# Kernel optimization log

Measured on AMD Instinct MI355X. Metric: run time of the kernel, lower is better.

Reference implementation:

```python
import jax, jax.numpy as jnp
import numpy as np

B, T, D = 64, 512, 512
H, DH = 8, 64  # head_num, att_embedding_size; H*DH == D
NEG = jnp.float32(-2.0**32 + 1)


def _pos_encoding(t, d):
    # Position_Embedding (mode='sum'): [cos, sin] concat over d/2 frequencies
    inv_freq = 1.0 / jnp.power(10000.0, 2.0 * jnp.arange(d // 2, dtype=jnp.float32) / d)
    pij = jnp.arange(t, dtype=jnp.float32)[:, None] * inv_freq[None, :]  # (T, d/2)
    return jnp.concatenate([jnp.cos(pij), jnp.sin(pij)], axis=-1)  # (T, d)


def setup_inputs() -> dict:
    key = jax.random.key(0)
    ks = jax.random.split(key, 9)
    queries = jax.random.normal(ks[0], (B, T, D), dtype=jnp.float32)
    keys = jax.random.normal(ks[1], (B, T, D), dtype=jnp.float32)
    query_lens = jax.random.randint(ks[2], (B, 1), 1, T + 1)
    key_lens = jax.random.randint(ks[3], (B, 1), 1, T + 1)
    W_Q = jax.random.truncated_normal(ks[4], -2., 2., (D, H * DH), dtype=jnp.float32) * 0.05
    W_K = jax.random.truncated_normal(ks[5], -2., 2., (D, H * DH), dtype=jnp.float32) * 0.05
    W_V = jax.random.truncated_normal(ks[6], -2., 2., (D, H * DH), dtype=jnp.float32) * 0.05
    fw1 = jax.random.normal(ks[7], (H * DH, 4 * H * DH), dtype=jnp.float32) * 0.02
    fw2 = jax.random.normal(ks[8], (4 * H * DH, H * DH), dtype=jnp.float32) * 0.02
    return {"queries": queries, "keys": keys, "query_lens": query_lens,
            "key_lens": key_lens, "W_Q": W_Q, "W_K": W_K, "W_V": W_V,
            "fw1": fw1, "fw2": fw2}


def reference(queries, keys, query_lens, key_lens, W_Q, W_K, W_V, fw1, fw2):
    # sequence masks (B, T) from lengths (B, 1)
    ar = jnp.arange(T)
    q_mask = (ar[None, :] < query_lens).astype(jnp.float32)  # (B, T)
    k_mask = ar[None, :] < key_lens                          # (B, T) bool

    pe = _pos_encoding(T, D)[None]  # (1, T, D)
    q_in = queries + pe
    k_in = keys + pe

    qp = jnp.einsum('btd,de->bte', q_in, W_Q).reshape(B, T, H, DH)
    kp = jnp.einsum('btd,de->bte', k_in, W_K)
    # DeepCTR quirk: values projected from the already-projected keys
    vp = jnp.einsum('btd,de->bte', kp, W_V).reshape(B, T, H, DH)
    kp = kp.reshape(B, T, H, DH)

    scores = jnp.einsum('bthd,bshd->bhts', qp, kp) / jnp.sqrt(jnp.float32(DH))
    scores = jnp.where(k_mask[:, None, None, :], scores, NEG)
    scores = scores - jnp.max(scores, axis=-1, keepdims=True)
    attn = jax.nn.softmax(scores, axis=-1)
    attn = attn * q_mask[:, None, :, None]

    out = jnp.einsum('bhts,bshd->bthd', attn, vp).reshape(B, T, H * DH)
    result = out + q_in  # residual uses PE-augmented queries

    ff = jnp.einsum('btd,df->btf', jax.nn.relu(jnp.einsum('btd,df->btf', result, fw1)), fw2)
    result = result + ff

    return jnp.mean(result, axis=1, keepdims=True)  # (B, 1, D)
```

## Files before the change

### kernel.cpp

```cpp
#include <hip/hip_runtime.h>

typedef unsigned short u16;
typedef __attribute__((ext_vector_type(8))) short short8;
typedef __attribute__((ext_vector_type(4))) float floatx4;

#define QSCALE 0.1803368801111204f

__device__ __forceinline__ u16 f2bf(float x) {
  union { float f; unsigned u; } un; un.f = x;
  unsigned r = un.u + 0x7fffu + ((un.u >> 16) & 1u);
  return (u16)(r >> 16);
}
__device__ __forceinline__ float bf2f(u16 h) {
  union { unsigned u; float f; } un; un.u = ((unsigned)h) << 16;
  return un.f;
}
__device__ __forceinline__ void gld16(const u16* g, u16* l) {
  __builtin_amdgcn_global_load_lds((__attribute__((address_space(1))) void*)g,
                                   (__attribute__((address_space(3))) void*)l, 16, 0, 0);
}

__global__ __launch_bounds__(256) void wtrans_all(const float* __restrict__ W_Q,
                                                  const float* __restrict__ W_K,
                                                  const float* __restrict__ fw1,
                                                  u16* __restrict__ WqT, u16* __restrict__ WkT,
                                                  u16* __restrict__ F1T) {
  __shared__ float tile[32][33];
  int L = blockIdx.x;
  const float* in;
  u16* out;
  int N, bx, by;
  if (L < 256) { in = W_Q; out = WqT; N = 512; bx = L & 15; by = L >> 4; }
  else if (L < 512) { L -= 256; in = W_K; out = WkT; N = 512; bx = L & 15; by = L >> 4; }
  else { L -= 512; in = fw1; out = F1T; N = 2048; bx = L & 63; by = L >> 6; }
  int tx = threadIdx.x, ty = threadIdx.y;
  int n0 = bx * 32, k0 = by * 32;
#pragma unroll
  for (int i = 0; i < 4; i++) {
    int kk = ty + i * 8;
    tile[kk][tx] = in[(size_t)(k0 + kk) * N + n0 + tx];
  }
  __syncthreads();
#pragma unroll
  for (int i = 0; i < 4; i++) {
    int nn = ty + i * 8;
    out[(size_t)(n0 + nn) * 512 + k0 + tx] = f2bf(tile[tx][nn]);
  }
}

__global__ __launch_bounds__(256) void wkv_kernel(const float* __restrict__ WK,
                                                  const float* __restrict__ WV,
                                                  u16* __restrict__ WkvT) {
  __shared__ float Kt[32][36];
  __shared__ float Vt[32][36];
  int nt = blockIdx.x & 15, dt = blockIdx.x >> 4;
  int n0 = nt * 32, d0 = dt * 32;
  int tid = threadIdx.x;
  int flat = tid * 4;
  int i4 = flat >> 5, j4 = flat & 31;
  int tn = tid & 15, td = tid >> 4;
  float acc00 = 0.f, acc01 = 0.f, acc10 = 0.f, acc11 = 0.f;
  for (int e0 = 0; e0 < 512; e0 += 32) {
    __syncthreads();
    *(float4*)&Kt[i4][j4] = *(const float4*)&WK[(size_t)(d0 + i4) * 512 + e0 + j4];
    *(float4*)&Vt[i4][j4] = *(const float4*)&WV[(size_t)(e0 + i4) * 512 + n0 + j4];
    __syncthreads();
#pragma unroll 8
    for (int e = 0; e < 32; e++) {
      float k0v = Kt[td * 2][e], k1v = Kt[td * 2 + 1][e];
      float v0 = Vt[e][tn * 2], v1 = Vt[e][tn * 2 + 1];
      acc00 += k0v * v0; acc01 += k0v * v1;
      acc10 += k1v * v0; acc11 += k1v * v1;
    }
  }
  size_t o = (size_t)(n0 + tn * 2) * 512 + d0 + td * 2;
  WkvT[o] = f2bf(acc00);
  WkvT[o + 1] = f2bf(acc10);
  WkvT[o + 512] = f2bf(acc01);
  WkvT[o + 513] = f2bf(acc11);
}

__global__ __launch_bounds__(256) void pe_table_kernel(float* __restrict__ pet) {
  int flat = (blockIdx.x * 256 + threadIdx.x) * 4;
  int d0 = flat & 511;
  int t = flat >> 9;
  float pe[4];
#pragma unroll
  for (int i = 0; i < 4; i++) {
    int d = d0 + i;
    int j = (d < 256) ? d : d - 256;
    float f = exp2f((float)j * -0.05190512648f);
    float arg = (float)t * f;
    pe[i] = (d < 256) ? cosf(arg) : sinf(arg);
  }
  *(float4*)(pet + flat) = *(const float4*)pe;
}

__global__ __launch_bounds__(256) void pe_add_kernel(const float* __restrict__ q,
                                                     const float* __restrict__ k,
                                                     const float* __restrict__ pet,
                                                     u16* __restrict__ qb, u16* __restrict__ kb) {
  size_t flat = ((size_t)blockIdx.x * 256 + threadIdx.x) * 4;
  const float4 qv = *(const float4*)(q + flat);
  const float4 kv = *(const float4*)(k + flat);
  const float4 pv = *(const float4*)(pet + (flat & 262143));
  u16 qo[4], ko[4];
  qo[0] = f2bf(qv.x + pv.x); qo[1] = f2bf(qv.y + pv.y);
  qo[2] = f2bf(qv.z + pv.z); qo[3] = f2bf(qv.w + pv.w);
  ko[0] = f2bf(kv.x + pv.x); ko[1] = f2bf(kv.y + pv.y);
  ko[2] = f2bf(kv.z + pv.z); ko[3] = f2bf(kv.w + pv.w);
  *(uint2*)(qb + flat) = *(const uint2*)qo;
  *(uint2*)(kb + flat) = *(const uint2*)ko;
}

template <int HT>
__device__ __forceinline__ void stage_half(const u16* M, int tbase, int k0, u16* buf,
                                           int w, int lane) {
  const int srow = lane >> 3;
  const int sg = (lane & 7) ^ srow;
#pragma unroll
  for (int i = 0; i < 2; i++) {
    int j = w * 2 + i;
    int row0;
    if constexpr (HT == 0) row0 = j * 8 + ((j >= 8) ? 64 : 0);
    else if constexpr (HT == 3) row0 = j * 8 + ((j >= 8) ? 64 : 0) + 64;
    else if constexpr (HT == 1) row0 = (j >> 2) * 64 + (j & 3) * 8;
    else row0 = (j >> 2) * 64 + 32 + (j & 3) * 8;
    gld16(M + ((size_t)(tbase + row0 + srow) * 512 + k0 + sg * 8), &buf[row0 * 64]);
  }
}

__device__ __forceinline__ void kloop256(const u16* __restrict__ A, const u16* __restrict__ Bt,
                                         int tm, int tn, u16* lds, int tid,
                                         floatx4 (&acc)[8][4]) {
  const int lane = tid & 63, w = tid >> 6;
  const int quad = lane >> 4, cl = lane & 15;
  const int wm = w >> 2, wn = w & 3;
  const int nk = 8;

  stage_half<0>(A, tm, 0, lds, w, lane);
  stage_half<1>(Bt, tn, 0, lds + 16384, w, lane);
  stage_half<2>(Bt, tn, 0, lds + 16384, w, lane);
  stage_half<3>(A, tm, 0, lds, w, lane);
  asm volatile("s_waitcnt vmcnt(4)" ::: "memory");
  __builtin_amdgcn_s_barrier();

#pragma unroll 1
  for (int kt = 0; kt < nk; kt++) {
    u16* Ab = lds + (kt & 1) * 32768;
    u16* Bb = Ab + 16384;
    u16* An = lds + ((kt & 1) ^ 1) * 32768;
    u16* Bn = An + 16384;
    const bool pf = (kt + 1 < nk);
    const int k0n = (kt + 1) << 6;
    short8 a0[4][2], a1[4][2], b0[2][2], b1[2][2];

#pragma unroll
    for (int f = 0; f < 4; f++)
#pragma unroll
      for (int kh = 0; kh < 2; kh++)
        a0[f][kh] = *(const short8*)&Ab[(wm * 128 + f * 16 + cl) * 64 + ((((kh << 2) + quad)) ^ (cl & 7)) * 8];
#pragma unroll
    for (int n = 0; n < 2; n++)
#pragma unroll
      for (int kh = 0; kh < 2; kh++)
        b0[n][kh] = *(const short8*)&Bb[(wn * 64 + n * 16 + cl) * 64 + ((((kh << 2) + quad)) ^ (cl & 7)) * 8];
    if (pf) {
      stage_half<0>(A, tm, k0n, An, w, lane);
      asm volatile("s_waitcnt vmcnt(4)" ::: "memory");
    } else {
      asm volatile("s_waitcnt vmcnt(2)" ::: "memory");
    }
    __builtin_amdgcn_s_barrier();
    asm volatile("s_waitcnt lgkmcnt(0)" ::: "memory");
    __builtin_amdgcn_sched_barrier(0);
    __builtin_amdgcn_s_setprio(1);
#pragma unroll
    for (int f = 0; f < 4; f++)
#pragma unroll
      for (int n = 0; n < 2; n++)
#pragma unroll
        for (int kh = 0; kh < 2; kh++)
          acc[f][n] = __builtin_amdgcn_mfma_f32_16x16x32_bf16(a0[f][kh], b0[n][kh], acc[f][n], 0, 0, 0);
    __builtin_amdgcn_s_setprio(0);
    __builtin_amdgcn_s_barrier();

#pragma unroll
    for (int n = 0; n < 2; n++)
#pragma unroll
      for (int kh = 0; kh < 2; kh++)
        b1[n][kh] = *(const short8*)&Bb[(wn * 64 + (n + 2) * 16 + cl) * 64 + ((((kh << 2) + quad)) ^ (cl & 7)) * 8];
    if (pf) {
      stage_half<1>(Bt, tn, k0n, Bn, w, lane);
      asm volatile("s_waitcnt vmcnt(4)" ::: "memory");
    } else {
      asm volatile("s_waitcnt vmcnt(0)" ::: "memory");
    }
    __builtin_amdgcn_s_barrier();
    asm volatile("s_waitcnt lgkmcnt(0)" ::: "memory");
    __builtin_amdgcn_sched_barrier(0);
    __builtin_amdgcn_s_setprio(1);
#pragma unroll
    for (int f = 0; f < 4; f++)
#pragma unroll
      for (int n = 0; n < 2; n++)
#pragma unroll
        for (int kh = 0; kh < 2; kh++)
          acc[f][n + 2] = __builtin_amdgcn_mfma_f32_16x16x32_bf16(a0[f][kh], b1[n][kh], acc[f][n + 2], 0, 0, 0);
    __builtin_amdgcn_s_setprio(0);
    __builtin_amdgcn_s_barrier();

#pragma unroll
    for (int f = 0; f < 4; f++)
#pragma unroll
      for (int kh = 0; kh < 2; kh++)
        a1[f][kh] = *(const short8*)&Ab[(wm * 128 + (f + 4) * 16 + cl) * 64 + ((((kh << 2) + quad)) ^ (cl & 7)) * 8];
    if (pf) stage_half<2>(Bt, tn, k0n, Bn, w, lane);
    __builtin_amdgcn_s_barrier();
    asm volatile("s_waitcnt lgkmcnt(0)" ::: "memory");
    __builtin_amdgcn_sched_barrier(0);
    __builtin_amdgcn_s_setprio(1);
#pragma unroll
    for (int f = 0; f < 4; f++)
#pragma unroll
      for (int n = 0; n < 2; n++)
#pragma unroll
        for (int kh = 0; kh < 2; kh++)
          acc[f + 4][n + 2] = __builtin_amdgcn_mfma_f32_16x16x32_bf16(a1[f][kh], b1[n][kh], acc[f + 4][n + 2], 0, 0, 0);
    __builtin_amdgcn_s_setprio(0);
    __builtin_amdgcn_s_barrier();

    if (pf) {
      stage_half<3>(A, tm, k0n, An, w, lane);
      asm volatile("s_waitcnt vmcnt(4)" ::: "memory");
    }
    __builtin_amdgcn_s_barrier();
    __builtin_amdgcn_s_setprio(1);
#pragma unroll
    for (int f = 0; f < 4; f++)
#pragma unroll
      for (int n = 0; n < 2; n++)
#pragma unroll
        for (int kh = 0; kh < 2; kh++)
          acc[f + 4][n] = __builtin_amdgcn_mfma_f32_16x16x32_bf16(a1[f][kh], b0[n][kh], acc[f + 4][n], 0, 0, 0);
    __builtin_amdgcn_s_setprio(0);
    __builtin_amdgcn_s_barrier();
  }
}

__global__ __launch_bounds__(512, 2) void proj_256(const u16* __restrict__ q_in,
                                                   const u16* __restrict__ k_in,
                                                   const u16* __restrict__ WqT,
                                                   const u16* __restrict__ WkT,
                                                   const u16* __restrict__ WkvT,
                                                   u16* __restrict__ qp,
                                                   u16* __restrict__ kpb,
                                                   u16* __restrict__ vTp) {
  __shared__ u16 lds[65536];
  const int tid = threadIdx.x;
  const int lane = tid & 63, w = tid >> 6;
  const int quad = lane >> 4, cl = lane & 15;
  const int wm = w >> 2, wn = w & 3;
  int L = blockIdx.x;
  const int seg = L >> 8;
  L &= 255;
  const u16* A = (seg == 0) ? q_in : k_in;
  const u16* Bt = (seg == 0) ? WqT : (seg == 1) ? WkT : WkvT;
  const int xcd = L & 7, s = L >> 3;
  const int nx = s & 1;
  const int rgrp = s >> 1;
  const int tm = (rgrp * 8 + xcd) * 256;
  const int tn = nx * 256;

  floatx4 acc[8][4] = {};
  kloop256(A, Bt, tm, tn, lds, tid, acc);

  if (seg < 2) {
    u16* C = (seg == 0) ? qp : kpb;
#pragma unroll
    for (int f = 0; f < 8; f++)
#pragma unroll
      for (int n = 0; n < 4; n++)
#pragma unroll
        for (int r = 0; r < 4; r++) {
          int row = tm + wm * 128 + f * 16 + quad * 4 + r;
          int col = tn + wn * 64 + n * 16 + cl;
          C[(size_t)row * 512 + col] = f2bf(acc[f][n][r]);
        }
  } else {
    const int b = tm >> 9, sbase = tm & 511;
#pragma unroll 1
    for (int p = 0; p < 2; p++) {
      __syncthreads();
      if ((wn >> 1) == p) {
        int cbase = (wn & 1) * 64;
#pragma unroll
        for (int f = 0; f < 8; f++)
#pragma unroll
          for (int n = 0; n < 4; n++)
#pragma unroll
            for (int r = 0; r < 4; r++) {
              int tc = cbase + n * 16 + cl;
              int row = wm * 128 + f * 16 + quad * 4 + r;
              lds[tc * 264 + row] = f2bf(acc[f][n][r]);
            }
      }
      __syncthreads();
      int col = tid >> 2;
      int e = tn + p * 128 + col;
      int h = e >> 6, d = e & 63;
      u16* dst = vTp + ((size_t)((b * 8 + h) * 64 + d) * 512 + sbase);
#pragma unroll
      for (int j = 0; j < 8; j++) {
        int chunk = (tid & 3) + j * 4;
        *(short8*)(dst + chunk * 8) = *(const short8*)&lds[col * 264 + chunk * 8];
      }
    }
  }
}

__global__ __launch_bounds__(512, 2) void ffn1_256(const u16* __restrict__ A,
                                                   const u16* __restrict__ Bt,
                                                   float* __restrict__ outp) {
  __shared__ u16 lds[65536];
  const int tid = threadIdx.x;
  const int lane = tid & 63, w = tid >> 6;
  const int quad = lane >> 4, cl = lane & 15;
  const int wn = w & 3;
  int L = blockIdx.x;
  const int xcd = L & 7, s = L >> 3;
  const int nx = s & 7;
  const int rgrp = s >> 3;
  const int tm = (rgrp * 8 + xcd) * 256;
  const int tn = nx * 256;

  floatx4 acc[8][4] = {};
  kloop256(A, Bt, tm, tn, lds, tid, acc);

  float cs[4] = {0.f, 0.f, 0.f, 0.f};
#pragma unroll
  for (int f = 0; f < 8; f++)
#pragma unroll
    for (int n = 0; n < 4; n++)
#pragma unroll
      for (int r = 0; r < 4; r++) cs[n] += fmaxf(acc[f][n][r], 0.0f);
#pragma unroll
  for (int n = 0; n < 4; n++) {
    cs[n] += __shfl_xor(cs[n], 16);
    cs[n] += __shfl_xor(cs[n], 32);
  }
  if (quad == 0) {
    int b = tm >> 9;
#pragma unroll
    for (int n = 0; n < 4; n++)
      atomicAdd(outp + (size_t)b * 2048 + tn + wn * 64 + n * 16 + cl, cs[n]);
  }
}

__global__ __launch_bounds__(256) void ffn2_mean_kernel(const float* __restrict__ sums,
                                                        const float* __restrict__ fw2,
                                                        float* __restrict__ outp) {
  __shared__ float s[128];
  int fs = blockIdx.x & 15, b = blockIdx.x >> 4;
  int tid = threadIdx.x;
  if (tid < 128) s[tid] = sums[(size_t)b * 2048 + fs * 128 + tid];
  __syncthreads();
  const float* w = fw2 + (size_t)(fs * 128) * 512;
  float a0 = 0.f, a1 = 0.f;
#pragma unroll 4
  for (int f = 0; f < 128; f++) {
    float sv = s[f];
    a0 += sv * w[(size_t)f * 512 + tid];
    a1 += sv * w[(size_t)f * 512 + 256 + tid];
  }
  atomicAdd(outp + b * 512 + tid, a0 * (1.0f / 512.0f));
  atomicAdd(outp + b * 512 + 256 + tid, a1 * (1.0f / 512.0f));
}

__global__ __launch_bounds__(256) void attn_kernel(const u16* __restrict__ qp, const u16* __restrict__ kp,
                                                   const u16* __restrict__ vT, const u16* __restrict__ qin,
                                                   u16* __restrict__ resout, const int* __restrict__ qlen,
                                                   const int* __restrict__ klen, float* __restrict__ outp) {
  __shared__ u16 KPu[8704];
  __shared__ u16 Vlds[64 * 128];
  __shared__ float Csum[4][64];
  int L = blockIdx.x;
  int xcd = L & 7;
  int idx = L >> 3;
  int qt = idx & 7;
  int g = xcd + (idx >> 3) * 8;
  int h = g & 7, b = g >> 3;
  int tid = threadIdx.x, lane = tid & 63, w = tid >> 6;
  int quad = lane >> 4, cl = lane & 15;
  int kl = klen[b], ql = qlen[b];
  int q0 = qt * 64 + w * 16;

  if (qt * 64 >= ql) {
    int c = tid & 63, r0 = (tid >> 6) * 16;
    float sv = 0.f;
#pragma unroll
    for (int i = 0; i < 16; i++) {
      size_t idx2 = ((size_t)(b * 512 + qt * 64 + r0 + i) * 512) + h * 64 + c;
      u16 val = qin[idx2];
      resout[idx2] = val;
      sv += bf2f(val);
    }
    Csum[w][c] = sv;
    __syncthreads();
    if (tid < 64) {
      float t = Csum[0][tid] + Csum[1][tid] + Csum[2][tid] + Csum[3][tid];
      atomicAdd(outp + b * 512 + h * 64 + tid, t * (1.0f / 512.0f));
    }
    return;
  }
  bool wactive = q0 < ql;

  short8 qfrag[2];
#pragma unroll
  for (int ks = 0; ks < 2; ks++)
    qfrag[ks] = *(const short8*)(qp + ((size_t)(b * 512 + q0 + cl) * 512 + h * 64 + ks * 32 + quad * 8));
  const short8 ones8 = {(short)0x3F80, (short)0x3F80, (short)0x3F80, (short)0x3F80,
                        (short)0x3F80, (short)0x3F80, (short)0x3F80, (short)0x3F80};
  float m_r[4];
  floatx4 o[4] = {};
  floatx4 lacc = {};
#pragma unroll
  for (int r = 0; r < 4; r++) m_r[r] = -3.0e38f;

  int nkt = (kl + 127) >> 7;
  for (int kt = 0; kt < nkt; kt++) {
    __syncthreads();
#pragma unroll
    for (int i = 0; i < 4; i++) {
      int c = w * 4 + i;
      int row = c * 8 + (lane >> 3);
      int gc = (lane & 7) ^ (row & 7);
      gld16(kp + ((size_t)(b * 512 + kt * 128 + row) * 512 + h * 64 + gc * 8), &KPu[c * 512]);
    }
#pragma unroll
    for (int i = 0; i < 4; i++) {
      int c = w * 4 + i;
      int row = c * 4 + (lane >> 4);
      int gc = (lane & 15) ^ (row & 7);
      gld16(vT + ((size_t)((b * 8 + h) * 64 + row) * 512 + kt * 128 + gc * 8), &Vlds[c * 512]);
    }
    asm volatile("s_waitcnt vmcnt(4)" ::: "memory");
    __builtin_amdgcn_s_barrier();
    __builtin_amdgcn_sched_barrier(0);
    floatx4 sacc[8] = {};
    float mnew[4], alpha[4];
    if (wactive) {
      __builtin_amdgcn_s_setprio(1);
#pragma unroll
      for (int f = 0; f < 8; f++) {
        int krow = f * 16 + cl;
#pragma unroll
        for (int ks = 0; ks < 2; ks++) {
          int kc = ks * 4 + quad;
          short8 kf = *(const short8*)&KPu[krow * 64 + ((kc ^ (cl & 7)) * 8)];
          sacc[f] = __builtin_amdgcn_mfma_f32_16x16x32_bf16(qfrag[ks], kf, sacc[f], 0, 0, 0);
        }
      }
      __builtin_amdgcn_s_setprio(0);
#pragma unroll
      for (int r = 0; r < 4; r++) mnew[r] = m_r[r];
#pragma unroll
      for (int f = 0; f < 8; f++) {
        int key = kt * 128 + f * 16 + cl;
        bool ok = key < kl;
#pragma unroll
        for (int r = 0; r < 4; r++) {
          float v = ok ? sacc[f][r] * QSCALE : -4294967296.0f;
          sacc[f][r] = v;
          mnew[r] = fmaxf(mnew[r], v);
        }
      }
#pragma unroll
      for (int mk = 1; mk <= 8; mk <<= 1)
#pragma unroll
        for (int r = 0; r < 4; r++) mnew[r] = fmaxf(mnew[r], __shfl_xor(mnew[r], mk));
#pragma unroll
      for (int r = 0; r < 4; r++) {
        alpha[r] = exp2f(m_r[r] - mnew[r]);
        m_r[r] = mnew[r];
      }
    }
    __syncthreads();
    if (wactive) {
      u16* P = &KPu[w * 2176];
#pragma unroll
      for (int f = 0; f < 8; f++)
#pragma unroll
        for (int r = 0; r < 4; r++) {
          float p = exp2f(sacc[f][r] - mnew[r]);
          P[(quad * 4 + r) * 136 + f * 16 + cl] = f2bf(p);
        }
#pragma unroll
      for (int r = 0; r < 4; r++) lacc[r] *= alpha[r];
#pragma unroll
      for (int fd = 0; fd < 4; fd++)
#pragma unroll
        for (int r = 0; r < 4; r++) o[fd][r] *= alpha[r];
      __builtin_amdgcn_s_setprio(1);
#pragma unroll
      for (int k2 = 0; k2 < 4; k2++) {
        short8 pf = *(const short8*)&P[cl * 136 + k2 * 32 + quad * 8];
        lacc = __builtin_amdgcn_mfma_f32_16x16x32_bf16(pf, ones8, lacc, 0, 0, 0);
#pragma unroll
        for (int fd = 0; fd < 4; fd++) {
          int vrow = fd * 16 + cl;
          int sc = k2 * 4 + quad;
          short8 vf = *(const short8*)&Vlds[vrow * 128 + ((sc ^ (cl & 7)) * 8)];
          o[fd] = __builtin_amdgcn_mfma_f32_16x16x32_bf16(pf, vf, o[fd], 0, 0, 0);
        }
      }
      __builtin_amdgcn_s_setprio(0);
    }
  }
  float colsum[4] = {0.f, 0.f, 0.f, 0.f};
#pragma unroll
  for (int fd = 0; fd < 4; fd++)
#pragma unroll
    for (int r = 0; r < 4; r++) {
      int q = q0 + quad * 4 + r;
      float v = o[fd][r] / lacc[r];
      if (q >= ql) v = 0.f;
      size_t idx2 = (size_t)(b * 512 + q) * 512 + h * 64 + fd * 16 + cl;
      v += bf2f(qin[idx2]);
      resout[idx2] = f2bf(v);
      colsum[fd] += v;
    }
#pragma unroll
  for (int fd = 0; fd < 4; fd++) {
    colsum[fd] += __shfl_xor(colsum[fd], 16);
    colsum[fd] += __shfl_xor(colsum[fd], 32);
  }
  if (quad == 0) {
#pragma unroll
    for (int fd = 0; fd < 4; fd++) Csum[w][fd * 16 + cl] = colsum[fd];
  }
  __syncthreads();
  if (tid < 64) {
    float t = Csum[0][tid] + Csum[1][tid] + Csum[2][tid] + Csum[3][tid];
    atomicAdd(outp + b * 512 + h * 64 + tid, t * (1.0f / 512.0f));
  }
}

extern "C" void kernel_launch(void* const* d_in, const int* in_sizes, int n_in,
                              void* d_out, int out_size, void* d_ws, size_t ws_size,
                              hipStream_t stream) {
  const float* queries = (const float*)d_in[0];
  const float* keys = (const float*)d_in[1];
  const int* qlen = (const int*)d_in[2];
  const int* klen = (const int*)d_in[3];
  const float* W_Q = (const float*)d_in[4];
  const float* W_K = (const float*)d_in[5];
  const float* W_V = (const float*)d_in[6];
  const float* fw1 = (const float*)d_in[7];
  const float* fw2 = (const float*)d_in[8];
  float* outp = (float*)d_out;
  char* ws = (char*)d_ws;

  constexpr size_t SZ_W = 512 * 512 * 2;
  constexpr size_t SZ_F = 2048 * 512 * 2;
  constexpr size_t SZ_S = 64 * 2048 * 4;
  constexpr size_t SZ_T = (size_t)64 * 512 * 512 * 2;
  size_t o_WqT = 0;
  size_t o_WkT = o_WqT + SZ_W;
  size_t o_Wkv = o_WkT + SZ_W;
  size_t o_F1T = o_Wkv + SZ_W;
  size_t o_SUM = o_F1T + SZ_F;
  size_t o_ABCD = o_SUM + SZ_S;
  size_t o_E = o_ABCD + 4 * SZ_T;
  size_t NEED = o_E + SZ_T;
  if (ws_size < NEED) return;

  u16* WqT = (u16*)(ws + o_WqT);
  u16* WkT = (u16*)(ws + o_WkT);
  u16* WkvT = (u16*)(ws + o_Wkv);
  u16* F1T = (u16*)(ws + o_F1T);
  float* sums = (float*)(ws + o_SUM);
  u16* q_in = (u16*)(ws + o_ABCD);
  u16* k_in = (u16*)(ws + o_ABCD + SZ_T);
  u16* qp = (u16*)(ws + o_ABCD + 2 * SZ_T);
  u16* kpb = (u16*)(ws + o_ABCD + 3 * SZ_T);
  u16* vT = (u16*)(ws + o_E);
  float* pet = (float*)(ws + o_E);
  u16* resb = k_in;

  hipMemsetAsync(d_out, 0, (size_t)out_size * sizeof(float), stream);
  hipMemsetAsync(sums, 0, SZ_S, stream);

  wtrans_all<<<1536, dim3(32, 8), 0, stream>>>(W_Q, W_K, fw1, WqT, WkT, F1T);
  wkv_kernel<<<256, 256, 0, stream>>>(W_K, W_V, WkvT);
  pe_table_kernel<<<256, 256, 0, stream>>>(pet);
  pe_add_kernel<<<16384, 256, 0, stream>>>(queries, keys, pet, q_in, k_in);

  proj_256<<<768, 512, 0, stream>>>(q_in, k_in, WqT, WkT, WkvT, qp, kpb, vT);

  attn_kernel<<<4096, 256, 0, stream>>>(qp, kpb, vT, q_in, resb, qlen, klen, outp);

  ffn1_256<<<1024, 512, 0, stream>>>(resb, F1T, sums);
  ffn2_mean_kernel<<<1024, 256, 0, stream>>>(sums, fw2, outp);
}
```

Baseline: 397.0 us.

## Merge prep kernels, simplify GEMM pipeline, replace atomics with deterministic reductions

Folds the weight transpose, Wk·Wv product and positional table into one prep kernel, cutting launches. The two memsets go away because attention and ffn1 now write per-tile partial sums to dedicated slots instead of accumulating with atomics. A single ffn2_final kernel reduces those slots, multiplies by fw2 and writes the output directly. The GEMM k-loop is restructured to prefetch the whole next A/B tile at once, dropping the staged quarter-loads and setprio. The cost is fewer barriers overlapping loads with MFMA, and a 64-block final kernel with little parallelism.

```diff
diff --git a/kernel.cpp b/kernel.cpp
--- a/kernel.cpp
+++ b/kernel.cpp
@@ -20,80 +20,80 @@
                                    (__attribute__((address_space(3))) void*)l, 16, 0, 0);
 }
 
-__global__ __launch_bounds__(256) void wtrans_all(const float* __restrict__ W_Q,
-                                                  const float* __restrict__ W_K,
-                                                  const float* __restrict__ fw1,
-                                                  u16* __restrict__ WqT, u16* __restrict__ WkT,
-                                                  u16* __restrict__ F1T) {
-  __shared__ float tile[32][33];
+__global__ __launch_bounds__(256) void prep_kernel(const float* __restrict__ W_Q,
+                                                   const float* __restrict__ W_K,
+                                                   const float* __restrict__ W_V,
+                                                   const float* __restrict__ fw1,
+                                                   u16* __restrict__ WqT, u16* __restrict__ WkT,
+                                                   u16* __restrict__ F1T, u16* __restrict__ WkvT,
+                                                   float* __restrict__ pet) {
   int L = blockIdx.x;
-  const float* in;
-  u16* out;
-  int N, bx, by;
-  if (L < 256) { in = W_Q; out = WqT; N = 512; bx = L & 15; by = L >> 4; }
-  else if (L < 512) { L -= 256; in = W_K; out = WkT; N = 512; bx = L & 15; by = L >> 4; }
-  else { L -= 512; in = fw1; out = F1T; N = 2048; bx = L & 63; by = L >> 6; }
-  int tx = threadIdx.x, ty = threadIdx.y;
-  int n0 = bx * 32, k0 = by * 32;
-#pragma unroll
-  for (int i = 0; i < 4; i++) {
-    int kk = ty + i * 8;
-    tile[kk][tx] = in[(size_t)(k0 + kk) * N + n0 + tx];
-  }
-  __syncthreads();
-#pragma unroll
-  for (int i = 0; i < 4; i++) {
-    int nn = ty + i * 8;
-    out[(size_t)(n0 + nn) * 512 + k0 + tx] = f2bf(tile[tx][nn]);
-  }
-}
-
-__global__ __launch_bounds__(256) void wkv_kernel(const float* __restrict__ WK,
-                                                  const float* __restrict__ WV,
-                                                  u16* __restrict__ WkvT) {
-  __shared__ float Kt[32][36];
-  __shared__ float Vt[32][36];
-  int nt = blockIdx.x & 15, dt = blockIdx.x >> 4;
-  int n0 = nt * 32, d0 = dt * 32;
-  int tid = threadIdx.x;
-  int flat = tid * 4;
-  int i4 = flat >> 5, j4 = flat & 31;
-  int tn = tid & 15, td = tid >> 4;
-  float acc00 = 0.f, acc01 = 0.f, acc10 = 0.f, acc11 = 0.f;
-  for (int e0 = 0; e0 < 512; e0 += 32) {
+  int tid = threadIdx.y * 32 + threadIdx.x;
+  if (L < 1536) {
+    __shared__ float tile[32][33];
+    const float* in;
+    u16* out;
+    int N, bx, by;
+    if (L < 256) { in = W_Q; out = WqT; N = 512; bx = L & 15; by = L >> 4; }
+    else if (L < 512) { L -= 256; in = W_K; out = WkT; N = 512; bx = L & 15; by = L >> 4; }
+    else { L -= 512; in = fw1; out = F1T; N = 2048; bx = L & 63; by = L >> 6; }
+    int tx = threadIdx.x, ty = threadIdx.y;
+    int n0 = bx * 32, k0 = by * 32;
+#pragma unroll
+    for (int i = 0; i < 4; i++) {
+      int kk = ty + i * 8;
+      tile[kk][tx] = in[(size_t)(k0 + kk) * N + n0 + tx];
+    }
     __syncthreads();
-    *(float4*)&Kt[i4][j4] = *(const float4*)&WK[(size_t)(d0 + i4) * 512 + e0 + j4];
-    *(float4*)&Vt[i4][j4] = *(const float4*)&WV[(size_t)(e0 + i4) * 512 + n0 + j4];
-    __syncthreads();
+#pragma unroll
+    for (int i = 0; i < 4; i++) {
+      int nn = ty + i * 8;
+      out[(size_t)(n0 + nn) * 512 + k0 + tx] = f2bf(tile[tx][nn]);
+    }
+  } else if (L < 1792) {
+    L -= 1536;
+    __shared__ float Kt[32][36];
+    __shared__ float Vt[32][36];
+    int nt = L & 15, dt = L >> 4;
+    int n0 = nt * 32, d0 = dt * 32;
+    int flat = tid * 4;
+    int i4 = flat >> 5, j4 = flat & 31;
+    int tn = tid & 15, td = tid >> 4;
+    float acc00 = 0.f, acc01 = 0.f, acc10 = 0.f, acc11 = 0.f;
+    for (int e0 = 0; e0 < 512; e0 += 32) {
+      __syncthreads();
+      *(float4*)&Kt[i4][j4] = *(const float4*)&W_K[(size_t)(d0 + i4) * 512 + e0 + j4];
+      *(float4*)&Vt[i4][j4] = *(const float4*)&W_V[(size_t)(e0 + i4) * 512 + n0 + j4];
+      __syncthreads();
 #pragma unroll 8
-    for (int e = 0; e < 32; e++) {
-      float k0v = Kt[td * 2][e], k1v = Kt[td * 2 + 1][e];
-      float v0 = Vt[e][tn * 2], v1 = Vt[e][tn * 2 + 1];
-      acc00 += k0v * v0; acc01 += k0v * v1;
-      acc10 += k1v * v0; acc11 += k1v * v1;
-    }
-  }
-  size_t o = (size_t)(n0 + tn * 2) * 512 + d0 + td * 2;
-  WkvT[o] = f2bf(acc00);
-  WkvT[o + 1] = f2bf(acc10);
-  WkvT[o + 512] = f2bf(acc01);
-  WkvT[o + 513] = f2bf(acc11);
-}
-
-__global__ __launch_bounds__(256) void pe_table_kernel(float* __restrict__ pet) {
-  int flat = (blockIdx.x * 256 + threadIdx.x) * 4;
-  int d0 = flat & 511;
-  int t = flat >> 9;
-  float pe[4];
-#pragma unroll
-  for (int i = 0; i < 4; i++) {
-    int d = d0 + i;
-    int j = (d < 256) ? d : d - 256;
-    float f = exp2f((float)j * -0.05190512648f);
-    float arg = (float)t * f;
-    pe[i] = (d < 256) ? cosf(arg) : sinf(arg);
-  }
-  *(float4*)(pet + flat) = *(const float4*)pe;
+      for (int e = 0; e < 32; e++) {
+        float k0v = Kt[td * 2][e], k1v = Kt[td * 2 + 1][e];
+        float v0 = Vt[e][tn * 2], v1 = Vt[e][tn * 2 + 1];
+        acc00 += k0v * v0; acc01 += k0v * v1;
+        acc10 += k1v * v0; acc11 += k1v * v1;
+      }
+    }
+    size_t o = (size_t)(n0 + tn * 2) * 512 + d0 + td * 2;
+    WkvT[o] = f2bf(acc00);
+    WkvT[o + 1] = f2bf(acc10);
+    WkvT[o + 512] = f2bf(acc01);
+    WkvT[o + 513] = f2bf(acc11);
+  } else {
+    L -= 1792;
+    int flat = (L * 256 + tid) * 4;
+    int d0 = flat & 511;
+    int t = flat >> 9;
+    float pe[4];
+#pragma unroll
+    for (int i = 0; i < 4; i++) {
+      int d = d0 + i;
+      int j = (d < 256) ? d : d - 256;
+      float f = exp2f((float)j * -0.05190512648f);
+      float arg = (float)t * f;
+      pe[i] = (d < 256) ? cosf(arg) : sinf(arg);
+    }
+    *(float4*)(pet + flat) = *(const float4*)pe;
+  }
 }
 
 __global__ __launch_bounds__(256) void pe_add_kernel(const float* __restrict__ q,
@@ -113,38 +113,33 @@
   *(uint2*)(kb + flat) = *(const uint2*)ko;
 }
 
-template <int HT>
-__device__ __forceinline__ void stage_half(const u16* M, int tbase, int k0, u16* buf,
-                                           int w, int lane) {
-  const int srow = lane >> 3;
-  const int sg = (lane & 7) ^ srow;
-#pragma unroll
-  for (int i = 0; i < 2; i++) {
-    int j = w * 2 + i;
-    int row0;
-    if constexpr (HT == 0) row0 = j * 8 + ((j >= 8) ? 64 : 0);
-    else if constexpr (HT == 3) row0 = j * 8 + ((j >= 8) ? 64 : 0) + 64;
-    else if constexpr (HT == 1) row0 = (j >> 2) * 64 + (j & 3) * 8;
-    else row0 = (j >> 2) * 64 + 32 + (j & 3) * 8;
-    gld16(M + ((size_t)(tbase + row0 + srow) * 512 + k0 + sg * 8), &buf[row0 * 64]);
-  }
-}
-
 __device__ __forceinline__ void kloop256(const u16* __restrict__ A, const u16* __restrict__ Bt,
                                          int tm, int tn, u16* lds, int tid,
                                          floatx4 (&acc)[8][4]) {
+  const int K = 512;
   const int lane = tid & 63, w = tid >> 6;
   const int quad = lane >> 4, cl = lane & 15;
   const int wm = w >> 2, wn = w & 3;
-  const int nk = 8;
-
-  stage_half<0>(A, tm, 0, lds, w, lane);
-  stage_half<1>(Bt, tn, 0, lds + 16384, w, lane);
-  stage_half<2>(Bt, tn, 0, lds + 16384, w, lane);
-  stage_half<3>(A, tm, 0, lds, w, lane);
-  asm volatile("s_waitcnt vmcnt(4)" ::: "memory");
-  __builtin_amdgcn_s_barrier();
-
+  const int srow = lane >> 3;
+  const int sg = (lane & 7) ^ srow;
+  const int cb = w * 4;
+
+  {
+    u16* Ab = lds;
+    u16* Bb = lds + 16384;
+#pragma unroll
+    for (int i = 0; i < 4; i++) {
+      int cc = cb + i, row = cc * 8 + srow;
+      gld16(A + ((size_t)(tm + row) * K + sg * 8), &Ab[cc * 512]);
+    }
+#pragma unroll
+    for (int i = 0; i < 4; i++) {
+      int cc = cb + i, row = cc * 8 + srow;
+      gld16(Bt + ((size_t)(tn + row) * K + sg * 8), &Bb[cc * 512]);
+    }
+  }
+
+  const int nk = K >> 6;
 #pragma unroll 1
   for (int kt = 0; kt < nk; kt++) {
     u16* Ab = lds + (kt & 1) * 32768;
@@ -153,8 +148,24 @@
     u16* Bn = An + 16384;
     const bool pf = (kt + 1 < nk);
     const int k0n = (kt + 1) << 6;
-    short8 a0[4][2], a1[4][2], b0[2][2], b1[2][2];
-
+    if (pf) {
+#pragma unroll
+      for (int i = 0; i < 4; i++) {
+        int cc = cb + i, row = cc * 8 + srow;
+        gld16(A + ((size_t)(tm + row) * K + k0n + sg * 8), &An[cc * 512]);
+      }
+#pragma unroll
+      for (int i = 0; i < 4; i++) {
+        int cc = cb + i, row = cc * 8 + srow;
+        gld16(Bt + ((size_t)(tn + row) * K + k0n + sg * 8), &Bn[cc * 512]);
+      }
+      asm volatile("s_waitcnt vmcnt(8)" ::: "memory");
+    } else {
+      asm volatile("s_waitcnt vmcnt(0)" ::: "memory");
+    }
+    __builtin_amdgcn_s_barrier();
+    __builtin_amdgcn_sched_barrier(0);
+    short8 a0[4][2], b0[2][2], b1[2][2], a1[4][2];
 #pragma unroll
     for (int f = 0; f < 4; f++)
 #pragma unroll
@@ -165,16 +176,6 @@
 #pragma unroll
       for (int kh = 0; kh < 2; kh++)
         b0[n][kh] = *(const short8*)&Bb[(wn * 64 + n * 16 + cl) * 64 + ((((kh << 2) + quad)) ^ (cl & 7)) * 8];
-    if (pf) {
-      stage_half<0>(A, tm, k0n, An, w, lane);
-      asm volatile("s_waitcnt vmcnt(4)" ::: "memory");
-    } else {
-      asm volatile("s_waitcnt vmcnt(2)" ::: "memory");
-    }
-    __builtin_amdgcn_s_barrier();
-    asm volatile("s_waitcnt lgkmcnt(0)" ::: "memory");
-    __builtin_amdgcn_sched_barrier(0);
-    __builtin_amdgcn_s_setprio(1);
 #pragma unroll
     for (int f = 0; f < 4; f++)
 #pragma unroll
@@ -182,24 +183,11 @@
 #pragma unroll
         for (int kh = 0; kh < 2; kh++)
           acc[f][n] = __builtin_amdgcn_mfma_f32_16x16x32_bf16(a0[f][kh], b0[n][kh], acc[f][n], 0, 0, 0);
-    __builtin_amdgcn_s_setprio(0);
-    __builtin_amdgcn_s_barrier();
-
 #pragma unroll
     for (int n = 0; n < 2; n++)
 #pragma unroll
       for (int kh = 0; kh < 2; kh++)
         b1[n][kh] = *(const short8*)&Bb[(wn * 64 + (n + 2) * 16 + cl) * 64 + ((((kh << 2) + quad)) ^ (cl & 7)) * 8];
-    if (pf) {
-      stage_half<1>(Bt, tn, k0n, Bn, w, lane);
-      asm volatile("s_waitcnt vmcnt(4)" ::: "memory");
-    } else {
-      asm volatile("s_waitcnt vmcnt(0)" ::: "memory");
-    }
-    __builtin_amdgcn_s_barrier();
-    asm volatile("s_waitcnt lgkmcnt(0)" ::: "memory");
-    __builtin_amdgcn_sched_barrier(0);
-    __builtin_amdgcn_s_setprio(1);
 #pragma unroll
     for (int f = 0; f < 4; f++)
 #pragma unroll
@@ -207,19 +195,11 @@
 #pragma unroll
         for (int kh = 0; kh < 2; kh++)
           acc[f][n + 2] = __builtin_amdgcn_mfma_f32_16x16x32_bf16(a0[f][kh], b1[n][kh], acc[f][n + 2], 0, 0, 0);
-    __builtin_amdgcn_s_setprio(0);
-    __builtin_amdgcn_s_barrier();
-
 #pragma unroll
     for (int f = 0; f < 4; f++)
 #pragma unroll
       for (int kh = 0; kh < 2; kh++)
         a1[f][kh] = *(const short8*)&Ab[(wm * 128 + (f + 4) * 16 + cl) * 64 + ((((kh << 2) + quad)) ^ (cl & 7)) * 8];
-    if (pf) stage_half<2>(Bt, tn, k0n, Bn, w, lane);
-    __builtin_amdgcn_s_barrier();
-    asm volatile("s_waitcnt lgkmcnt(0)" ::: "memory");
-    __builtin_amdgcn_sched_barrier(0);
-    __builtin_amdgcn_s_setprio(1);
 #pragma unroll
     for (int f = 0; f < 4; f++)
 #pragma unroll
@@ -227,15 +207,6 @@
 #pragma unroll
         for (int kh = 0; kh < 2; kh++)
           acc[f + 4][n + 2] = __builtin_amdgcn_mfma_f32_16x16x32_bf16(a1[f][kh], b1[n][kh], acc[f + 4][n + 2], 0, 0, 0);
-    __builtin_amdgcn_s_setprio(0);
-    __builtin_amdgcn_s_barrier();
-
-    if (pf) {
-      stage_half<3>(A, tm, k0n, An, w, lane);
-      asm volatile("s_waitcnt vmcnt(4)" ::: "memory");
-    }
-    __builtin_amdgcn_s_barrier();
-    __builtin_amdgcn_s_setprio(1);
 #pragma unroll
     for (int f = 0; f < 4; f++)
 #pragma unroll
@@ -243,7 +214,6 @@
 #pragma unroll
         for (int kh = 0; kh < 2; kh++)
           acc[f + 4][n] = __builtin_amdgcn_mfma_f32_16x16x32_bf16(a1[f][kh], b0[n][kh], acc[f + 4][n], 0, 0, 0);
-    __builtin_amdgcn_s_setprio(0);
     __builtin_amdgcn_s_barrier();
   }
 }
@@ -321,12 +291,12 @@
 
 __global__ __launch_bounds__(512, 2) void ffn1_256(const u16* __restrict__ A,
                                                    const u16* __restrict__ Bt,
-                                                   float* __restrict__ outp) {
+                                                   float* __restrict__ sums2) {
   __shared__ u16 lds[65536];
   const int tid = threadIdx.x;
   const int lane = tid & 63, w = tid >> 6;
   const int quad = lane >> 4, cl = lane & 15;
-  const int wn = w & 3;
+  const int wm = w >> 2, wn = w & 3;
   int L = blockIdx.x;
   const int xcd = L & 7, s = L >> 3;
   const int nx = s & 7;
@@ -349,38 +319,43 @@
     cs[n] += __shfl_xor(cs[n], 16);
     cs[n] += __shfl_xor(cs[n], 32);
   }
+  float* red = (float*)lds;
   if (quad == 0) {
-    int b = tm >> 9;
-#pragma unroll
-    for (int n = 0; n < 4; n++)
-      atomicAdd(outp + (size_t)b * 2048 + tn + wn * 64 + n * 16 + cl, cs[n]);
-  }
-}
-
-__global__ __launch_bounds__(256) void ffn2_mean_kernel(const float* __restrict__ sums,
-                                                        const float* __restrict__ fw2,
-                                                        float* __restrict__ outp) {
-  __shared__ float s[128];
-  int fs = blockIdx.x & 15, b = blockIdx.x >> 4;
-  int tid = threadIdx.x;
-  if (tid < 128) s[tid] = sums[(size_t)b * 2048 + fs * 128 + tid];
+#pragma unroll
+    for (int n = 0; n < 4; n++) red[wm * 256 + wn * 64 + n * 16 + cl] = cs[n];
+  }
   __syncthreads();
-  const float* w = fw2 + (size_t)(fs * 128) * 512;
-  float a0 = 0.f, a1 = 0.f;
-#pragma unroll 4
-  for (int f = 0; f < 128; f++) {
-    float sv = s[f];
-    a0 += sv * w[(size_t)f * 512 + tid];
-    a1 += sv * w[(size_t)f * 512 + 256 + tid];
-  }
-  atomicAdd(outp + b * 512 + tid, a0 * (1.0f / 512.0f));
-  atomicAdd(outp + b * 512 + 256 + tid, a1 * (1.0f / 512.0f));
+  if (tid < 256) {
+    int mtile = tm >> 8;
+    sums2[(size_t)mtile * 2048 + tn + tid] = red[tid] + red[256 + tid];
+  }
+}
+
+__global__ __launch_bounds__(512) void ffn2_final_kernel(const float* __restrict__ sums2,
+                                                         const float* __restrict__ attnacc,
+                                                         const float* __restrict__ fw2,
+                                                         float* __restrict__ outp) {
+  __shared__ float s[2048];
+  int b = blockIdx.x, col = threadIdx.x;
+  for (int i = col; i < 2048; i += 512)
+    s[i] = sums2[(size_t)(2 * b) * 2048 + i] + sums2[(size_t)(2 * b + 1) * 2048 + i];
+  __syncthreads();
+  const float* w = fw2 + col;
+  float a = 0.f;
+#pragma unroll 8
+  for (int f = 0; f < 2048; f++) a += s[f] * w[(size_t)f * 512];
+  int h = col >> 6, c = col & 63;
+  float att = 0.f;
+  const float* ap = attnacc + ((size_t)(b * 8 + h) * 8) * 64 + c;
+#pragma unroll
+  for (int qt = 0; qt < 8; qt++) att += ap[qt * 64];
+  outp[(size_t)b * 512 + col] = (a + att) * (1.0f / 512.0f);
 }
 
 __global__ __launch_bounds__(256) void attn_kernel(const u16* __restrict__ qp, const u16* __restrict__ kp,
                                                    const u16* __restrict__ vT, const u16* __restrict__ qin,
                                                    u16* __restrict__ resout, const int* __restrict__ qlen,
-                                                   const int* __restrict__ klen, float* __restrict__ outp) {
+                                                   const int* __restrict__ klen, float* __restrict__ attnacc) {
   __shared__ u16 KPu[8704];
   __shared__ u16 Vlds[64 * 128];
   __shared__ float Csum[4][64];
@@ -394,6 +369,7 @@
   int quad = lane >> 4, cl = lane & 15;
   int kl = klen[b], ql = qlen[b];
   int q0 = qt * 64 + w * 16;
+  float* aslot = attnacc + ((size_t)(g * 8 + qt)) * 64;
 
   if (qt * 64 >= ql) {
     int c = tid & 63, r0 = (tid >> 6) * 16;
@@ -407,10 +383,7 @@
     }
     Csum[w][c] = sv;
     __syncthreads();
-    if (tid < 64) {
-      float t = Csum[0][tid] + Csum[1][tid] + Csum[2][tid] + Csum[3][tid];
-      atomicAdd(outp + b * 512 + h * 64 + tid, t * (1.0f / 512.0f));
-    }
+    if (tid < 64) aslot[tid] = Csum[0][tid] + Csum[1][tid] + Csum[2][tid] + Csum[3][tid];
     return;
   }
   bool wactive = q0 < ql;
@@ -540,10 +513,7 @@
     for (int fd = 0; fd < 4; fd++) Csum[w][fd * 16 + cl] = colsum[fd];
   }
   __syncthreads();
-  if (tid < 64) {
-    float t = Csum[0][tid] + Csum[1][tid] + Csum[2][tid] + Csum[3][tid];
-    atomicAdd(outp + b * 512 + h * 64 + tid, t * (1.0f / 512.0f));
-  }
+  if (tid < 64) aslot[tid] = Csum[0][tid] + Csum[1][tid] + Csum[2][tid] + Csum[3][tid];
 }
 
 extern "C" void kernel_launch(void* const* d_in, const int* in_sizes, int n_in,
@@ -563,14 +533,16 @@
 
   constexpr size_t SZ_W = 512 * 512 * 2;
   constexpr size_t SZ_F = 2048 * 512 * 2;
-  constexpr size_t SZ_S = 64 * 2048 * 4;
+  constexpr size_t SZ_S = 128 * 2048 * 4;
+  constexpr size_t SZ_A = 4096 * 64 * 4;
   constexpr size_t SZ_T = (size_t)64 * 512 * 512 * 2;
   size_t o_WqT = 0;
   size_t o_WkT = o_WqT + SZ_W;
   size_t o_Wkv = o_WkT + SZ_W;
   size_t o_F1T = o_Wkv + SZ_W;
   size_t o_SUM = o_F1T + SZ_F;
-  size_t o_ABCD = o_SUM + SZ_S;
+  size_t o_ATT = o_SUM + SZ_S;
+  size_t o_ABCD = o_ATT + SZ_A;
   size_t o_E = o_ABCD + 4 * SZ_T;
   size_t NEED = o_E + SZ_T;
   if (ws_size < NEED) return;
@@ -579,7 +551,8 @@
   u16* WkT = (u16*)(ws + o_WkT);
   u16* WkvT = (u16*)(ws + o_Wkv);
   u16* F1T = (u16*)(ws + o_F1T);
-  float* sums = (float*)(ws + o_SUM);
+  float* sums2 = (float*)(ws + o_SUM);
+  float* attnacc = (float*)(ws + o_ATT);
   u16* q_in = (u16*)(ws + o_ABCD);
   u16* k_in = (u16*)(ws + o_ABCD + SZ_T);
   u16* qp = (u16*)(ws + o_ABCD + 2 * SZ_T);
@@ -588,18 +561,13 @@
   float* pet = (float*)(ws + o_E);
   u16* resb = k_in;
 
-  hipMemsetAsync(d_out, 0, (size_t)out_size * sizeof(float), stream);
-  hipMemsetAsync(sums, 0, SZ_S, stream);
-
-  wtrans_all<<<1536, dim3(32, 8), 0, stream>>>(W_Q, W_K, fw1, WqT, WkT, F1T);
-  wkv_kernel<<<256, 256, 0, stream>>>(W_K, W_V, WkvT);
-  pe_table_kernel<<<256, 256, 0, stream>>>(pet);
+  prep_kernel<<<2048, dim3(32, 8), 0, stream>>>(W_Q, W_K, W_V, fw1, WqT, WkT, F1T, WkvT, pet);
   pe_add_kernel<<<16384, 256, 0, stream>>>(queries, keys, pet, q_in, k_in);
 
   proj_256<<<768, 512, 0, stream>>>(q_in, k_in, WqT, WkT, WkvT, qp, kpb, vT);
 
-  attn_kernel<<<4096, 256, 0, stream>>>(qp, kpb, vT, q_in, resb, qlen, klen, outp);
-
-  ffn1_256<<<1024, 512, 0, stream>>>(resb, F1T, sums);
-  ffn2_mean_kernel<<<1024, 256, 0, stream>>>(sums, fw2, outp);
-}
+  attn_kernel<<<4096, 256, 0, stream>>>(qp, kpb, vT, q_in, resb, qlen, klen, attnacc);
+
+  ffn1_256<<<1024, 512, 0, stream>>>(resb, F1T, sums2);
+  ffn2_final_kernel<<<64, 512, 0, stream>>>(sums2, attnacc, fw2, outp);
+}
```

New measurement: 484.1 us. 21.9% more time.
